# Performance work log

Hardware: AMD Instinct MI355X
Metric: run time of the kernel (lower is better)

## Reference

```python
import jax, jax.numpy as jnp
import numpy as np

EPS = 1e-06


def rotation_trick(e, q):
    # e, q: (..., D). Faithful to torch version, but r_rT @ e and
    # q_hat_e_hatT @ e are algebraically simplified to r*(r.e) and
    # q_hat*(e_hat.e), avoiding the (..., D, D) outer-product tensors.
    sg = jax.lax.stop_gradient
    e_norm = sg(jnp.linalg.norm(e, axis=-1, keepdims=True)) + EPS
    q_norm = sg(jnp.linalg.norm(q, axis=-1, keepdims=True)) + EPS
    e_hat = sg(e / e_norm)
    q_hat = sg(q / q_norm)
    lmbda = q_norm / e_norm
    r = e_hat + q_hat
    r = r / jnp.linalg.norm(r, axis=-1, keepdims=True)
    r_dot_e = jnp.sum(r * e, axis=-1, keepdims=True)
    ehat_dot_e = jnp.sum(e_hat * e, axis=-1, keepdims=True)
    return lmbda * (e - 2.0 * r * r_dot_e + 2.0 * q_hat * ehat_dot_e)


def setup_inputs() -> dict:
    key = jax.random.key(0)
    k1, k2 = jax.random.split(key)
    B, D, H, W = 8, 64, 32, 32
    K = 8192
    x = jax.random.normal(k1, (B, D, H, W), dtype=jnp.float32)
    # init_tensor: L2-normalize uniform rand along dim=1, scale=1
    e = jax.random.uniform(k2, (D, K), dtype=jnp.float32)
    e_i_ts = e / (jnp.linalg.norm(e, axis=1, keepdims=True) + 1e-12)
    return {"x": x, "e_i_ts": e_i_ts}


def reference(x, e_i_ts):
    # x: (B, D, H, W); e_i_ts: (D, K)
    B, D, H, W = x.shape
    x_perm = jnp.transpose(x, (0, 2, 3, 1))          # (B, H, W, D)
    flat_x = x_perm.reshape(-1, D)                   # (N, D)
    distances = (
        jnp.sum(flat_x**2, axis=1, keepdims=True)
        - 2.0 * flat_x @ e_i_ts
        + jnp.sum(e_i_ts**2, axis=0, keepdims=True)
    )                                                # (N, K)
    encoding_indices = jnp.argmin(distances, axis=1) # (N,)
    ind = encoding_indices.reshape(B, H, W)
    quantized_x = e_i_ts.T[ind]                      # (B, H, W, D) gather
    quantized_x_d = rotation_trick(x_perm, quantized_x)
    # permute back to channels-first
    q = jnp.transpose(quantized_x, (0, 3, 1, 2))
    q_d = jnp.transpose(quantized_x_d, (0, 3, 1, 2))
    return (q_d, q, ind)
```

## Files before the change

kernel.cpp:

```cpp
#include <hip/hip_runtime.h>
#include <float.h>
#include <math.h>

#define EPS 1e-6f

typedef __attribute__((ext_vector_type(8))) short short8;
typedef __attribute__((ext_vector_type(4))) float f32x4;

constexpr int Nn = 8192;
constexpr int Dd = 64;
constexpr int Kk = 8192;
constexpr int PLANE = Nn * Dd;
constexpr int KSPLIT = 32;
constexpr int KPB = Kk / KSPLIT;
constexpr int NT = KPB / 16;
constexpr int TILE_USH = 6 * 64 * 8;

__device__ __forceinline__ void split3(float v, unsigned short& h1, unsigned short& h2, unsigned short& h3) {
    unsigned u = __float_as_uint(v);
    h1 = (unsigned short)(u >> 16);
    float r1 = v - __uint_as_float((unsigned)h1 << 16);
    h2 = (unsigned short)(__float_as_uint(r1) >> 16);
    float r2 = r1 - __uint_as_float((unsigned)h2 << 16);
    h3 = (unsigned short)(__float_as_uint(r2) >> 16);
}

__global__ void prep_kernel(const float* __restrict__ e, const float* __restrict__ x,
                            unsigned short* __restrict__ es_t, float* __restrict__ en2h,
                            float* __restrict__ et,
                            unsigned short* __restrict__ xs, float* __restrict__ xn2)
{
    const int tid = threadIdx.x;
    if (blockIdx.x < 32) {
        const int k = blockIdx.x * 256 + tid;
        const int t = k >> 4, l15 = k & 15;
        unsigned short* tb = es_t + (size_t)t * TILE_USH;
        float s = 0.f;
        #pragma unroll
        for (int c = 0; c < 8; ++c) {
            const int ks = c >> 2, kg = c & 3;
            short8 h1v, h2v, h3v;
            float fv[8];
            #pragma unroll
            for (int j = 0; j < 8; ++j) {
                float v = e[(c * 8 + j) * Kk + k];
                fv[j] = v;
                s = fmaf(v, v, s);
                unsigned short h1, h2, h3; split3(v, h1, h2, h3);
                h1v[j] = (short)h1; h2v[j] = (short)h2; h3v[j] = (short)h3;
            }
            const int lofs = (kg * 16 + l15) * 8;
            *(short8*)(tb + (0 * 2 + ks) * 512 + lofs) = h1v;
            *(short8*)(tb + (1 * 2 + ks) * 512 + lofs) = h2v;
            *(short8*)(tb + (2 * 2 + ks) * 512 + lofs) = h3v;
            *(float4*)(et + (size_t)k * Dd + c * 8)     = *(float4*)&fv[0];
            *(float4*)(et + (size_t)k * Dd + c * 8 + 4) = *(float4*)&fv[4];
        }
        en2h[k] = 0.5f * s;
    } else {
        const int p = (blockIdx.x - 32) * 256 + tid;
        const int b = p >> 10, hw = p & 1023;
        float s = 0.f;
        #pragma unroll
        for (int c = 0; c < 8; ++c) {
            short8 h1v, h2v, h3v;
            #pragma unroll
            for (int j = 0; j < 8; ++j) {
                float v = x[(b * Dd + c * 8 + j) * 1024 + hw];
                s = fmaf(v, v, s);
                unsigned short h1, h2, h3; split3(-v, h1, h2, h3);
                h1v[j] = (short)h1; h2v[j] = (short)h2; h3v[j] = (short)h3;
            }
            *(short8*)(xs + (size_t)p * Dd + c * 8) = h1v;
            *(short8*)(xs + PLANE + (size_t)p * Dd + c * 8) = h2v;
            *(short8*)(xs + 2 * PLANE + (size_t)p * Dd + c * 8) = h3v;
        }
        xn2[p] = s;
    }
}

__device__ __forceinline__ void tile_compute(
    const short8 (&a)[2][3][2], const short8 (&b)[6], float en,
    int nb, int l15, float (&bv)[2][4], int (&bi)[2][4])
{
    f32x4 acc[2][2];
    acc[0][0] = f32x4{en, en, en, en}; acc[1][0] = f32x4{en, en, en, en};
    acc[0][1] = f32x4{0.f, 0.f, 0.f, 0.f}; acc[1][1] = f32x4{0.f, 0.f, 0.f, 0.f};
    #define PROD(sx, se) \
        acc[0][0] = __builtin_amdgcn_mfma_f32_16x16x32_bf16(a[0][sx][0], b[(se)*2+0], acc[0][0], 0,0,0); \
        acc[1][0] = __builtin_amdgcn_mfma_f32_16x16x32_bf16(a[1][sx][0], b[(se)*2+0], acc[1][0], 0,0,0); \
        acc[0][1] = __builtin_amdgcn_mfma_f32_16x16x32_bf16(a[0][sx][1], b[(se)*2+1], acc[0][1], 0,0,0); \
        acc[1][1] = __builtin_amdgcn_mfma_f32_16x16x32_bf16(a[1][sx][1], b[(se)*2+1], acc[1][1], 0,0,0);
    PROD(0,0) PROD(0,1) PROD(1,0) PROD(0,2) PROD(1,1) PROD(2,0)
    #undef PROD
    #pragma unroll
    for (int mi = 0; mi < 2; ++mi)
        #pragma unroll
        for (int j = 0; j < 4; ++j) {
            float s = acc[mi][0][j] + acc[mi][1][j];
            if (s < bv[mi][j]) { bv[mi][j] = s; bi[mi][j] = nb + l15; }
        }
}

#define LOADB(bf, env, ti) { \
    const short8* tp_ = (const short8*)(es_t + (size_t)(ti) * TILE_USH) + lane; \
    bf[0] = tp_[0];   bf[1] = tp_[64];  bf[2] = tp_[128]; \
    bf[3] = tp_[192]; bf[4] = tp_[256]; bf[5] = tp_[320]; \
    env = en2h[(ti) * 16 + l15]; }

__global__ __launch_bounds__(256, 3) void dist_mfma(
    const unsigned short* __restrict__ xs, const unsigned short* __restrict__ es_t,
    const float* __restrict__ en2h,
    float* __restrict__ pval, int* __restrict__ pidx)
{
    const int tid = threadIdx.x;
    const int w = tid >> 6, lane = tid & 63;
    const int l15 = lane & 15, kg = lane >> 4;
    const int m0 = blockIdx.x * 128 + w * 32;
    const int t0 = blockIdx.y * NT;

    short8 a[2][3][2];
    #pragma unroll
    for (int mi = 0; mi < 2; ++mi) {
        const unsigned short* xp = xs + (size_t)(m0 + mi * 16 + l15) * Dd + kg * 8;
        #pragma unroll
        for (int s = 0; s < 3; ++s)
            #pragma unroll
            for (int ks = 0; ks < 2; ++ks)
                a[mi][s][ks] = *(const short8*)(xp + s * PLANE + ks * 32);
    }

    float bv[2][4]; int bi[2][4];
    #pragma unroll
    for (int mi = 0; mi < 2; ++mi)
        #pragma unroll
        for (int j = 0; j < 4; ++j) { bv[mi][j] = FLT_MAX; bi[mi][j] = 0; }

    short8 bA[6], bB[6]; float enA, enB;
    LOADB(bA, enA, t0)
    #pragma unroll 1
    for (int nt = 0; nt < NT; nt += 2) {
        const int ti = t0 + nt;
        LOADB(bB, enB, ti + 1)
        tile_compute(a, bA, enA, ti * 16, l15, bv, bi);
        if (nt + 2 < NT) { LOADB(bA, enA, ti + 2) }
        tile_compute(a, bB, enB, ti * 16 + 16, l15, bv, bi);
    }

    #pragma unroll
    for (int m = 1; m < 16; m <<= 1) {
        #pragma unroll
        for (int mi = 0; mi < 2; ++mi)
            #pragma unroll
            for (int j = 0; j < 4; ++j) {
                float ov = __shfl_xor(bv[mi][j], m, 64);
                int   oi = __shfl_xor(bi[mi][j], m, 64);
                if (ov < bv[mi][j] || (ov == bv[mi][j] && oi < bi[mi][j])) {
                    bv[mi][j] = ov; bi[mi][j] = oi;
                }
            }
    }
    if (l15 == 0) {
        #pragma unroll
        for (int mi = 0; mi < 2; ++mi)
            #pragma unroll
            for (int j = 0; j < 4; ++j) {
                int pix = m0 + mi * 16 + kg * 4 + j;
                pval[(size_t)pix * KSPLIT + blockIdx.y] = bv[mi][j];
                pidx[(size_t)pix * KSPLIT + blockIdx.y] = bi[mi][j];
            }
    }
}

__global__ __launch_bounds__(256) void finalize_kernel(
    const float* __restrict__ x, const float* __restrict__ et,
    const float* __restrict__ en2h, const float* __restrict__ xn2,
    const float* __restrict__ pval, const int* __restrict__ pidx,
    float* __restrict__ out_qd, float* __restrict__ out_q, float* __restrict__ out_ind)
{
    const int tid = threadIdx.x;
    const int p = blockIdx.x * 256 + tid;

    const float4* pv4 = (const float4*)(pval + (size_t)p * KSPLIT);
    const int4*   pi4 = (const int4*)(pidx + (size_t)p * KSPLIT);
    float bvv = FLT_MAX; int bii = 0;
    #pragma unroll
    for (int u = 0; u < KSPLIT / 4; ++u) {
        float4 v4 = pv4[u]; int4 i4 = pi4[u];
        #pragma unroll
        for (int jj = 0; jj < 4; ++jj) {
            float v = ((const float*)&v4)[jj];
            int   i = ((const int*)&i4)[jj];
            if (v < bvv || (v == bvv && i < bii)) { bvv = v; bii = i; }
        }
    }
    if (blockIdx.y == 0) out_ind[p] = (float)bii;

    float sx2 = xn2[p];
    float enh = en2h[bii];
    float sq2 = 2.f * enh;
    float sxq = enh - bvv;
    float ne = sqrtf(sx2), nq = sqrtf(sq2);
    float inv_e = 1.f / (ne + EPS), inv_q = 1.f / (nq + EPS);
    float lmbda = (nq + EPS) * inv_e;
    float ehat_dot_e = sx2 * inv_e;
    float rn2 = sx2 * inv_e * inv_e + 2.f * sxq * inv_e * inv_q + sq2 * inv_q * inv_q;
    float inv_r = rsqrtf(rn2);
    float rde = (sx2 * inv_e + sxq * inv_q) * inv_r;
    float cx = lmbda * (1.f - 2.f * rde * inv_r * inv_e);
    float cq = 2.f * lmbda * inv_q * (ehat_dot_e - rde * inv_r);

    const int b = p >> 10, hw = p & 1023;
    const int d0 = blockIdx.y * 32;
    const float* xb = x + (b * Dd + d0) * 1024 + hw;
    const float* er = et + (size_t)bii * Dd + d0;
    float* qd_b = out_qd + (b * Dd + d0) * 1024 + hw;
    float* q_b  = out_q  + (b * Dd + d0) * 1024 + hw;
    #pragma unroll
    for (int dv = 0; dv < 8; ++dv) {
        float4 q4 = *(const float4*)(er + dv * 4);
        #pragma unroll
        for (int jj = 0; jj < 4; ++jj) {
            int d = dv * 4 + jj;
            float xv = xb[d * 1024];
            float qv = ((const float*)&q4)[jj];
            qd_b[d * 1024] = cx * xv + cq * qv;
            q_b[d * 1024]  = qv;
        }
    }
}

extern "C" void kernel_launch(void* const* d_in, const int* in_sizes, int n_in,
                              void* d_out, int out_size, void* d_ws, size_t ws_size,
                              hipStream_t stream) {
    const float* x = (const float*)d_in[0];
    const float* e = (const float*)d_in[1];
    float* out = (float*)d_out;
    float* out_qd  = out;
    float* out_q   = out + Nn * Dd;
    float* out_ind = out + 2 * Nn * Dd;

    unsigned short* xs   = (unsigned short*)d_ws;
    unsigned short* es_t = xs + 3 * PLANE;
    float* et   = (float*)(es_t + (size_t)(Kk / 16) * TILE_USH);
    float* en2h = et + (size_t)Kk * Dd;
    float* xn2  = en2h + Kk;
    float* pval = xn2 + Nn;
    int*   pidx = (int*)(pval + (size_t)Nn * KSPLIT);

    prep_kernel<<<64, 256, 0, stream>>>(e, x, es_t, en2h, et, xs, xn2);
    dist_mfma<<<dim3(Nn / 128, KSPLIT), 256, 0, stream>>>(xs, es_t, en2h, pval, pidx);
    finalize_kernel<<<dim3(32, 2), 256, 0, stream>>>(x, et, en2h, xn2, pval, pidx,
                                                     out_qd, out_q, out_ind);
}
```

Baseline: 72.91 us.

## Halve K split, double-buffer two tiles per load, widen finalize grid

The distance kernel now splits K into 16 chunks instead of 32, so each block handles twice as many codewords. Codebook fragments are loaded two tiles at a time into 12-register buffers, with sched_barrier fences to keep loads ahead of the MFMA work. Launch bounds drop to 2 blocks per SM to make room for the extra registers. The finalize kernel is split over 8 channel groups instead of 2 to raise parallelism in the output writes, at the cost of recomputing the per-point argmin reduction and rotation coefficients in more blocks.

Measured after the change: 66.74 us. 1.09x faster.

```diff
diff --git a/kernel.cpp b/kernel.cpp
--- a/kernel.cpp
+++ b/kernel.cpp
@@ -11,7 +11,7 @@
 constexpr int Dd = 64;
 constexpr int Kk = 8192;
 constexpr int PLANE = Nn * Dd;
-constexpr int KSPLIT = 32;
+constexpr int KSPLIT = 16;
 constexpr int KPB = Kk / KSPLIT;
 constexpr int NT = KPB / 16;
 constexpr int TILE_USH = 6 * 64 * 8;
@@ -80,7 +80,7 @@
 }
 
 __device__ __forceinline__ void tile_compute(
-    const short8 (&a)[2][3][2], const short8 (&b)[6], float en,
+    const short8 (&a)[2][3][2], const short8* b, float en,
     int nb, int l15, float (&bv)[2][4], int (&bi)[2][4])
 {
     f32x4 acc[2][2];
@@ -102,13 +102,15 @@
         }
 }
 
-#define LOADB(bf, env, ti) { \
-    const short8* tp_ = (const short8*)(es_t + (size_t)(ti) * TILE_USH) + lane; \
-    bf[0] = tp_[0];   bf[1] = tp_[64];  bf[2] = tp_[128]; \
-    bf[3] = tp_[192]; bf[4] = tp_[256]; bf[5] = tp_[320]; \
-    env = en2h[(ti) * 16 + l15]; }
-
-__global__ __launch_bounds__(256, 3) void dist_mfma(
+#define LOADB2(bf, e0, e1, ti) { \
+    const short8* p0_ = (const short8*)(es_t + (size_t)(ti) * TILE_USH) + lane; \
+    bf[0] = p0_[0];   bf[1] = p0_[64];  bf[2]  = p0_[128]; \
+    bf[3] = p0_[192]; bf[4] = p0_[256]; bf[5]  = p0_[320]; \
+    bf[6] = p0_[384]; bf[7] = p0_[448]; bf[8]  = p0_[512]; \
+    bf[9] = p0_[576]; bf[10] = p0_[640]; bf[11] = p0_[704]; \
+    e0 = en2h[(ti) * 16 + l15]; e1 = en2h[(ti) * 16 + 16 + l15]; }
+
+__global__ __launch_bounds__(256, 2) void dist_mfma(
     const unsigned short* __restrict__ xs, const unsigned short* __restrict__ es_t,
     const float* __restrict__ en2h,
     float* __restrict__ pval, int* __restrict__ pidx)
@@ -136,15 +138,22 @@
         #pragma unroll
         for (int j = 0; j < 4; ++j) { bv[mi][j] = FLT_MAX; bi[mi][j] = 0; }
 
-    short8 bA[6], bB[6]; float enA, enB;
-    LOADB(bA, enA, t0)
+    short8 bA[12], bB[12]; float enA0, enA1, enB0, enB1;
+    LOADB2(bA, enA0, enA1, t0)
+    __builtin_amdgcn_sched_barrier(0);
     #pragma unroll 1
-    for (int nt = 0; nt < NT; nt += 2) {
-        const int ti = t0 + nt;
-        LOADB(bB, enB, ti + 1)
-        tile_compute(a, bA, enA, ti * 16, l15, bv, bi);
-        if (nt + 2 < NT) { LOADB(bA, enA, ti + 2) }
-        tile_compute(a, bB, enB, ti * 16 + 16, l15, bv, bi);
+    for (int j = 0; j < NT / 4; ++j) {
+        const int ti = t0 + j * 4;
+        LOADB2(bB, enB0, enB1, ti + 2)
+        __builtin_amdgcn_sched_barrier(0);
+        tile_compute(a, &bA[0], enA0, (ti + 0) * 16, l15, bv, bi);
+        tile_compute(a, &bA[6], enA1, (ti + 1) * 16, l15, bv, bi);
+        if (j + 1 < NT / 4) {
+            LOADB2(bA, enA0, enA1, ti + 4)
+            __builtin_amdgcn_sched_barrier(0);
+        }
+        tile_compute(a, &bB[0], enB0, (ti + 2) * 16, l15, bv, bi);
+        tile_compute(a, &bB[6], enB1, (ti + 3) * 16, l15, bv, bi);
     }
 
     #pragma unroll
@@ -211,13 +220,13 @@
     float cq = 2.f * lmbda * inv_q * (ehat_dot_e - rde * inv_r);
 
     const int b = p >> 10, hw = p & 1023;
-    const int d0 = blockIdx.y * 32;
+    const int d0 = blockIdx.y * 8;
     const float* xb = x + (b * Dd + d0) * 1024 + hw;
     const float* er = et + (size_t)bii * Dd + d0;
     float* qd_b = out_qd + (b * Dd + d0) * 1024 + hw;
     float* q_b  = out_q  + (b * Dd + d0) * 1024 + hw;
     #pragma unroll
-    for (int dv = 0; dv < 8; ++dv) {
+    for (int dv = 0; dv < 2; ++dv) {
         float4 q4 = *(const float4*)(er + dv * 4);
         #pragma unroll
         for (int jj = 0; jj < 4; ++jj) {
@@ -250,6 +259,6 @@
 
     prep_kernel<<<64, 256, 0, stream>>>(e, x, es_t, en2h, et, xs, xn2);
     dist_mfma<<<dim3(Nn / 128, KSPLIT), 256, 0, stream>>>(xs, es_t, en2h, pval, pidx);
-    finalize_kernel<<<dim3(32, 2), 256, 0, stream>>>(x, et, en2h, xn2, pval, pidx,
+    finalize_kernel<<<dim3(32, 8), 256, 0, stream>>>(x, et, en2h, xn2, pval, pidx,
                                                      out_qd, out_q, out_ind);
 }
```

## Stage codebook tiles in LDS via async global-to-LDS loads, fewer K splits

Applied to the files above, without the earlier changes.

The distance kernel now double-buffers pairs of codebook tiles in shared memory using global_load_lds, so all four waves share one copy instead of each wave loading the tiles from global memory itself. The K split drops from 32 to 8, so each block scans more codewords and fewer partial results are written, and the launch bound goes from 3 to 2 blocks per CU. The finalize kernel is regridded to 8 blocks along D, each covering 8 channels, for more parallelism. The risks are a __syncthreads on every iteration, lower occupancy, and a dist grid of only 512 blocks for 256 CUs.

Result: faster. 64.12 us (-12.1%).

```diff
diff --git a/kernel.cpp b/kernel.cpp
--- a/kernel.cpp
+++ b/kernel.cpp
@@ -11,10 +11,12 @@
 constexpr int Dd = 64;
 constexpr int Kk = 8192;
 constexpr int PLANE = Nn * Dd;
-constexpr int KSPLIT = 32;
+constexpr int KSPLIT = 8;
 constexpr int KPB = Kk / KSPLIT;
 constexpr int NT = KPB / 16;
+constexpr int NPAIR = NT / 2;
 constexpr int TILE_USH = 6 * 64 * 8;
+constexpr int TILE_BYTES = TILE_USH * 2;
 
 __device__ __forceinline__ void split3(float v, unsigned short& h1, unsigned short& h2, unsigned short& h3) {
     unsigned u = __float_as_uint(v);
@@ -23,6 +25,12 @@
     h2 = (unsigned short)(__float_as_uint(r1) >> 16);
     float r2 = r1 - __uint_as_float((unsigned)h2 << 16);
     h3 = (unsigned short)(__float_as_uint(r2) >> 16);
+}
+
+typedef __attribute__((address_space(3))) unsigned int lds_u32_t;
+typedef __attribute__((address_space(1))) unsigned int glb_u32_t;
+__device__ __forceinline__ void gload_lds16(const void* g, void* l) {
+    __builtin_amdgcn_global_load_lds((const glb_u32_t*)g, (lds_u32_t*)l, 16, 0, 0);
 }
 
 __global__ void prep_kernel(const float* __restrict__ e, const float* __restrict__ x,
@@ -102,17 +110,13 @@
         }
 }
 
-#define LOADB(bf, env, ti) { \
-    const short8* tp_ = (const short8*)(es_t + (size_t)(ti) * TILE_USH) + lane; \
-    bf[0] = tp_[0];   bf[1] = tp_[64];  bf[2] = tp_[128]; \
-    bf[3] = tp_[192]; bf[4] = tp_[256]; bf[5] = tp_[320]; \
-    env = en2h[(ti) * 16 + l15]; }
-
-__global__ __launch_bounds__(256, 3) void dist_mfma(
+__global__ __launch_bounds__(256, 2) void dist_mfma(
     const unsigned short* __restrict__ xs, const unsigned short* __restrict__ es_t,
     const float* __restrict__ en2h,
     float* __restrict__ pval, int* __restrict__ pidx)
 {
+    __shared__ __align__(16) unsigned short sB[2][2 * TILE_USH];
+
     const int tid = threadIdx.x;
     const int w = tid >> 6, lane = tid & 63;
     const int l15 = lane & 15, kg = lane >> 4;
@@ -136,15 +140,38 @@
         #pragma unroll
         for (int j = 0; j < 4; ++j) { bv[mi][j] = FLT_MAX; bi[mi][j] = 0; }
 
-    short8 bA[6], bB[6]; float enA, enB;
-    LOADB(bA, enA, t0)
+    #define STAGE_PAIR(buf, pi) { \
+        const char* gb_ = (const char*)es_t + (size_t)(pi) * (2 * TILE_BYTES); \
+        char* lb_ = (char*)&sB[buf][0]; \
+        _Pragma("unroll") \
+        for (int r_ = 0; r_ < 3; ++r_) { \
+            const int off_ = r_ * 4096 + w * 1024; \
+            gload_lds16(gb_ + off_ + lane * 16, lb_ + off_); } }
+
+    STAGE_PAIR(0, t0 / 2)
+    __syncthreads();
+
     #pragma unroll 1
-    for (int nt = 0; nt < NT; nt += 2) {
-        const int ti = t0 + nt;
-        LOADB(bB, enB, ti + 1)
-        tile_compute(a, bA, enA, ti * 16, l15, bv, bi);
-        if (nt + 2 < NT) { LOADB(bA, enA, ti + 2) }
-        tile_compute(a, bB, enB, ti * 16 + 16, l15, bv, bi);
+    for (int p = 0; p < NPAIR; ++p) {
+        const int cur = p & 1;
+        if (p + 1 < NPAIR) { STAGE_PAIR(cur ^ 1, t0 / 2 + p + 1) }
+
+        const int ti = t0 + p * 2;
+        float en0 = en2h[ti * 16 + l15];
+        float en1 = en2h[ti * 16 + 16 + l15];
+
+        short8 bf0[6], bf1[6];
+        {
+            const unsigned short* lb = &sB[cur][lane * 8];
+            #pragma unroll
+            for (int f = 0; f < 6; ++f) bf0[f] = *(const short8*)(lb + f * 512);
+            #pragma unroll
+            for (int f = 0; f < 6; ++f) bf1[f] = *(const short8*)(lb + TILE_USH + f * 512);
+        }
+        tile_compute(a, bf0, en0, ti * 16, l15, bv, bi);
+        tile_compute(a, bf1, en1, ti * 16 + 16, l15, bv, bi);
+
+        __syncthreads();
     }
 
     #pragma unroll
@@ -211,13 +238,13 @@
     float cq = 2.f * lmbda * inv_q * (ehat_dot_e - rde * inv_r);
 
     const int b = p >> 10, hw = p & 1023;
-    const int d0 = blockIdx.y * 32;
+    const int d0 = blockIdx.y * 8;
     const float* xb = x + (b * Dd + d0) * 1024 + hw;
     const float* er = et + (size_t)bii * Dd + d0;
     float* qd_b = out_qd + (b * Dd + d0) * 1024 + hw;
     float* q_b  = out_q  + (b * Dd + d0) * 1024 + hw;
     #pragma unroll
-    for (int dv = 0; dv < 8; ++dv) {
+    for (int dv = 0; dv < 2; ++dv) {
         float4 q4 = *(const float4*)(er + dv * 4);
         #pragma unroll
         for (int jj = 0; jj < 4; ++jj) {
@@ -250,6 +277,6 @@
 
     prep_kernel<<<64, 256, 0, stream>>>(e, x, es_t, en2h, et, xs, xn2);
     dist_mfma<<<dim3(Nn / 128, KSPLIT), 256, 0, stream>>>(xs, es_t, en2h, pval, pidx);
-    finalize_kernel<<<dim3(32, 2), 256, 0, stream>>>(x, et, en2h, xn2, pval, pidx,
+    finalize_kernel<<<dim3(32, 8), 256, 0, stream>>>(x, et, en2h, xn2, pval, pidx,
                                                      out_qd, out_q, out_ind);
 }
```
